# Kernel optimization log

Measured on AMD Instinct MI355X. Metric: run time of the kernel, lower is better.

## Reference

```python
import jax, jax.numpy as jnp
import numpy as np

B, N, D, H, L = 1024, 31, 576, 16, 12   # batch, tokens (30 patches + cls), dim, heads, depth
DH = D // H        # 36 head dim
FF = 4 * D         # 2304 mlp hidden
NC = 1000          # num_classes
EPS = 1e-5         # torch nn.LayerNorm default
NEG = -987654321.0 # exact constant used for the LSA diagonal mask


def layer_norm(x, w, b):
    m = jnp.mean(x, axis=-1, keepdims=True)
    v = jnp.mean((x - m) ** 2, axis=-1, keepdims=True)
    return (x - m) * jax.lax.rsqrt(v + EPS) * w + b


def setup_inputs() -> dict:
    key = jax.random.key(0)
    ks = jax.random.split(key, 12)
    s = 0.02
    return {
        "x": jax.random.normal(ks[0], (B, N, D), jnp.float32),
        # per-layer stacked params (scanned over depth L)
        "qkv_w": jax.random.normal(ks[1], (L, 3 * D, D), jnp.float32) * s,
        "scale": (DH ** -0.5) * jnp.ones((L, H), jnp.float32),  # learnable per-head LSA scale
        "out_w": jax.random.normal(ks[2], (L, D, D), jnp.float32) * s,
        "out_b": jnp.zeros((L, D), jnp.float32),
        "ln1_w": jnp.ones((L, D), jnp.float32),
        "ln1_b": jnp.zeros((L, D), jnp.float32),
        "ln2_w": jnp.ones((L, D), jnp.float32),
        "ln2_b": jnp.zeros((L, D), jnp.float32),
        "fc1_w": jax.random.normal(ks[3], (L, FF, D), jnp.float32) * s,
        "fc1_b": jnp.zeros((L, FF), jnp.float32),
        "fc2_w": jax.random.normal(ks[4], (L, D, FF), jnp.float32) * s,
        "fc2_b": jnp.zeros((L, D), jnp.float32),
        "norm_w": jnp.ones((D,), jnp.float32),
        "norm_b": jnp.zeros((D,), jnp.float32),
        "head_w": jax.random.normal(ks[5], (NC, D), jnp.float32) * s,
        "head_b": jnp.zeros((NC,), jnp.float32),
    }


def reference(x, qkv_w, scale, out_w, out_b, ln1_w, ln1_b, ln2_w, ln2_b,
              fc1_w, fc1_b, fc2_w, fc2_b, norm_w, norm_b, head_w, head_b):
    diag = jnp.eye(N, dtype=bool)  # LSA diagonal mask (self-token)

    def block(h, p):
        qw, sc, ow, ob, w1, b1, w2, b2, g1, be1, g2, be2 = p
        # --- LSA attention ---
        y = layer_norm(h, g1, be1)
        qkv = jnp.einsum('bnd,ed->bne', y, qw)            # [B,N,3D]
        q, k, v = jnp.split(qkv, 3, axis=-1)
        to_heads = lambda t: t.reshape(t.shape[0], N, H, DH).transpose(0, 2, 1, 3)
        q, k, v = to_heads(q), to_heads(k), to_heads(v)   # [B,H,N,DH]
        dots = jnp.einsum('bhid,bhjd->bhij', q, k) * sc[None, :, None, None]
        dots = jnp.where(diag, NEG, dots)                 # diagonal -> -987654321
        attn = jax.nn.softmax(dots, axis=-1)
        o = jnp.einsum('bhij,bhjd->bhid', attn, v)
        o = o.transpose(0, 2, 1, 3).reshape(h.shape[0], N, D)
        h = h + jnp.einsum('bnd,ed->bne', o, ow) + ob
        # --- MLP (exact GELU) ---
        y = layer_norm(h, g2, be2)
        m = jax.nn.gelu(jnp.einsum('bnd,fd->bnf', y, w1) + b1, approximate=False)
        h = h + jnp.einsum('bnf,df->bnd', m, w2) + b2
        return h, None

    params = (qkv_w, scale, out_w, out_b, fc1_w, fc1_b, fc2_w, fc2_b,
              ln1_w, ln1_b, ln2_w, ln2_b)
    x, _ = jax.lax.scan(block, x, params)
    x = layer_norm(x, norm_w, norm_b)
    cls = x[:, 0]                                         # cls token
    return cls @ head_w.T + head_b                        # [B, NC]
```

## Files before the change

kernel.cpp:

```cpp
#include <hip/hip_runtime.h>
#include <stdint.h>

typedef unsigned short u16;
typedef __bf16 bf16x8 __attribute__((ext_vector_type(8)));
typedef float f32x4 __attribute__((ext_vector_type(4)));

#define B_   1024
#define N_   31
#define D_   576
#define H_   16
#define L_   12
#define DH_  36
#define FF_  2304
#define NC_  1000
#define M_   (B_*N_)
#define NEG_ (-987654321.0f)

__device__ __forceinline__ u16 f2bfbits(float f) {
  uint32_t x = __builtin_bit_cast(uint32_t, f);
  x += 0x7fffu + ((x >> 16) & 1u);
  return (u16)(x >> 16);
}
__device__ __forceinline__ float bfbits2f(u16 u) {
  return __builtin_bit_cast(float, (uint32_t)u << 16);
}
__device__ __forceinline__ float lo_bf(uint32_t w) {
  return __builtin_bit_cast(float, w << 16);
}
__device__ __forceinline__ float hi_bf(uint32_t w) {
  return __builtin_bit_cast(float, w & 0xffff0000u);
}

typedef __attribute__((address_space(1))) void gvoid_t;
typedef __attribute__((address_space(3))) void lvoid_t;
__device__ __forceinline__ void async16(void* lds, const void* g) {
  __builtin_amdgcn_global_load_lds((gvoid_t*)const_cast<void*>(g), (lvoid_t*)lds, 16, 0, 0);
}

template<int EPI>
__global__ __launch_bounds__(256, 3)
void gemm_bt(const u16* __restrict__ A, const u16* __restrict__ Bw,
             int N, int K,
             const float* __restrict__ bias,
             float* __restrict__ resid,
             u16* __restrict__ outb,
             float* __restrict__ outf, int Nreal)
{
  __shared__ alignas(16) u16 As[256 * 32];
  __shared__ alignas(16) u16 Bs[64 * 32];

  const int t    = threadIdx.x;
  const int wave = t >> 6;
  const int lane = t & 63;

  const int nwg  = gridDim.x * gridDim.y;
  const int orig = blockIdx.y * gridDim.x + blockIdx.x;
  const int q = nwg >> 3, r = nwg & 7, xc = orig & 7, o = orig >> 3;
  const int wid = (xc < r ? xc * (q + 1) : r * (q + 1) + (xc - r) * q) + o;
  const int mBase = (wid / gridDim.x) * 256;
  const int nBase = (wid % gridDim.x) * 64;

  const int tr = t >> 2;
  const int tc = (t & 3) * 8;

  const int fr = lane & 15;
  const int fk = (lane >> 4) * 8;
  const u16* aBase = &As[(wave * 64 + fr) * 32 + fk];
  const u16* bBase = &Bs[fr * 32 + fk];

  f32x4 acc[4][4] = {};

  for (int k0 = 0; k0 < K; k0 += 32) {
    #pragma unroll
    for (int i = 0; i < 4; ++i) {
      int row = i * 64 + tr;
      async16(&As[row * 32 + tc], A + (long)(mBase + row) * K + k0 + tc);
    }
    async16(&Bs[tr * 32 + tc], Bw + (long)(nBase + tr) * K + k0 + tc);
    asm volatile("s_waitcnt vmcnt(0)" ::: "memory");
    __syncthreads();

    bf16x8 af[4], bf_[4];
    #pragma unroll
    for (int m = 0; m < 4; ++m) af[m]  = *(const bf16x8*)(aBase + m * 16 * 32);
    #pragma unroll
    for (int n = 0; n < 4; ++n) bf_[n] = *(const bf16x8*)(bBase + n * 16 * 32);
    #pragma unroll
    for (int m = 0; m < 4; ++m)
      #pragma unroll
      for (int n = 0; n < 4; ++n)
        acc[m][n] = __builtin_amdgcn_mfma_f32_16x16x32_bf16(af[m], bf_[n], acc[m][n], 0, 0, 0);
    __syncthreads();
  }

  const int fq = lane >> 4;
  #pragma unroll
  for (int m = 0; m < 4; ++m) {
    int gr0 = mBase + wave * 64 + m * 16 + fq * 4;
    #pragma unroll
    for (int n = 0; n < 4; ++n) {
      int gc = nBase + n * 16 + fr;
      #pragma unroll
      for (int r2 = 0; r2 < 4; ++r2) {
        long gr = gr0 + r2;
        float v = acc[m][n][r2];
        if (EPI == 0) {
          outb[gr * N + gc] = f2bfbits(v);
        } else if (EPI == 1) {
          long idx = gr * N + gc;
          resid[idx] = resid[idx] + v + bias[gc];
        } else if (EPI == 2) {
          float x = v + bias[gc];
          float g = 0.5f * x * (1.0f + erff(x * 0.70710678118654752f));
          outb[gr * N + gc] = f2bfbits(g);
        } else {
          if (gc < Nreal) outf[gr * Nreal + gc] = v + bias[gc];
        }
      }
    }
  }
}

__global__ __launch_bounds__(256)
void ln_kernel(const float* __restrict__ x, long tokStride,
               const float* __restrict__ w, const float* __restrict__ b,
               u16* __restrict__ y)
{
  int tok  = blockIdx.x * 4 + (threadIdx.x >> 6);
  int lane = threadIdx.x & 63;
  const float* row = x + (long)tok * tokStride;
  float v[9]; float s = 0.f, sq = 0.f;
  #pragma unroll
  for (int j = 0; j < 9; ++j) { v[j] = row[lane + j * 64]; s += v[j]; sq += v[j] * v[j]; }
  #pragma unroll
  for (int o = 32; o; o >>= 1) { s += __shfl_xor(s, o); sq += __shfl_xor(sq, o); }
  float mean = s * (1.f / 576.f);
  float var  = sq * (1.f / 576.f) - mean * mean;
  float inv  = rsqrtf(var + 1e-5f);
  u16* yr = y + (long)tok * 576;
  #pragma unroll
  for (int j = 0; j < 9; ++j) {
    int c = lane + j * 64;
    yr[c] = f2bfbits((v[j] - mean) * inv * w[c] + b[c]);
  }
}

__global__ __launch_bounds__(256)
void attn_kernel(const u16* __restrict__ qkv, u16* __restrict__ o,
                 const float* __restrict__ scale)
{
  __shared__ float kls[4][N_ * DH_];
  __shared__ float vls[4][N_ * DH_];
  int wave = threadIdx.x >> 6, lane = threadIdx.x & 63;
  int bh = blockIdx.x * 4 + wave;
  int b  = bh >> 4, h = bh & 15;
  long base = (long)b * N_ * 1728 + h * DH_;

  for (int u = lane; u < 558; u += 64) {
    int row = u / 18, c = (u % 18) * 2;
    uint32_t kw = *(const uint32_t*)(qkv + base + 576  + (long)row * 1728 + c);
    uint32_t vw = *(const uint32_t*)(qkv + base + 1152 + (long)row * 1728 + c);
    kls[wave][row * 36 + c]     = lo_bf(kw);
    kls[wave][row * 36 + c + 1] = hi_bf(kw);
    vls[wave][row * 36 + c]     = lo_bf(vw);
    vls[wave][row * 36 + c + 1] = hi_bf(vw);
  }
  __syncthreads();

  int i0 = lane >> 1, p = lane & 1;
  int i  = i0 > 30 ? 30 : i0;
  float qv[18];
  const u16* qrow = qkv + base + (long)i * 1728 + p * 18;
  #pragma unroll
  for (int d = 0; d < 18; ++d) qv[d] = bfbits2f(qrow[d]);

  float s[31];
  #pragma unroll
  for (int j = 0; j < 31; ++j) {
    float a = 0.f;
    const float* kr = &kls[wave][j * 36 + p * 18];
    #pragma unroll
    for (int d = 0; d < 18; ++d) a += qv[d] * kr[d];
    a += __shfl_xor(a, 1);
    s[j] = a;
  }
  float sc = scale[h];
  float mx = -1e30f;
  #pragma unroll
  for (int j = 0; j < 31; ++j) { s[j] = (j == i) ? NEG_ : s[j] * sc; mx = fmaxf(mx, s[j]); }
  float sum = 0.f;
  #pragma unroll
  for (int j = 0; j < 31; ++j) { s[j] = expf(s[j] - mx); sum += s[j]; }
  float inv = 1.f / sum;

  #pragma unroll
  for (int d = 0; d < 18; ++d) {
    float a = 0.f;
    #pragma unroll
    for (int j = 0; j < 31; ++j) a += s[j] * vls[wave][j * 36 + p * 18 + d];
    if (i0 < 31)
      o[(long)(b * N_ + i0) * 576 + h * DH_ + p * 18 + d] = f2bfbits(a * inv);
  }
}

__global__ void cvt_layer(const float4* __restrict__ s0, const float4* __restrict__ s1,
                          const float4* __restrict__ s2, const float4* __restrict__ s3,
                          u16* __restrict__ d0, u16* __restrict__ d1,
                          u16* __restrict__ d2, u16* __restrict__ d3)
{
  int idx = blockIdx.x * 256 + threadIdx.x;
  const float4* s; u16* d; int off;
  if (idx < 248832)      { s = s0; d = d0; off = idx; }
  else if (idx < 331776) { s = s1; d = d1; off = idx - 248832; }
  else if (idx < 663552) { s = s2; d = d2; off = idx - 331776; }
  else                   { s = s3; d = d3; off = idx - 663552; }
  float4 v = s[off];
  ushort4 r;
  r.x = f2bfbits(v.x); r.y = f2bfbits(v.y); r.z = f2bfbits(v.z); r.w = f2bfbits(v.w);
  *(ushort4*)(d + (long)off * 4) = r;
}

__global__ void pad_head(const float* __restrict__ hw, u16* __restrict__ out)
{
  int idx = blockIdx.x * 256 + threadIdx.x;
  int row = idx / 576;
  out[idx] = (row < NC_) ? f2bfbits(hw[idx]) : (u16)0;
}

extern "C" void kernel_launch(void* const* d_in, const int* in_sizes, int n_in,
                              void* d_out, int out_size, void* d_ws, size_t ws_size,
                              hipStream_t stream)
{
  (void)in_sizes; (void)n_in; (void)out_size;
  const float* x      = (const float*)d_in[0];
  const float* qkv_w  = (const float*)d_in[1];
  const float* scale  = (const float*)d_in[2];
  const float* out_w  = (const float*)d_in[3];
  const float* out_b  = (const float*)d_in[4];
  const float* ln1_w  = (const float*)d_in[5];
  const float* ln1_b  = (const float*)d_in[6];
  const float* ln2_w  = (const float*)d_in[7];
  const float* ln2_b  = (const float*)d_in[8];
  const float* fc1_w  = (const float*)d_in[9];
  const float* fc1_b  = (const float*)d_in[10];
  const float* fc2_w  = (const float*)d_in[11];
  const float* fc2_b  = (const float*)d_in[12];
  const float* norm_w = (const float*)d_in[13];
  const float* norm_b = (const float*)d_in[14];
  const float* head_w = (const float*)d_in[15];
  const float* head_b = (const float*)d_in[16];

  auto al = [](size_t b) { return (b + 255) & ~(size_t)255; };
  const size_t fixed = al((size_t)M_ * D_ * 4) + al((size_t)M_ * D_ * 2)
                     + al((size_t)1728 * D_ * 2) + al((size_t)D_ * D_ * 2)
                     + al((size_t)FF_ * D_ * 2) + al((size_t)D_ * FF_ * 2)
                     + 2 * al((size_t)1024 * D_ * 2);
  const size_t cbuf2 = al((size_t)(M_ / 2) * FF_ * 2);
  const int nch = (ws_size >= fixed + cbuf2) ? 2 : 4;
  const int MC  = M_ / nch;
  const int BCc = B_ / nch;

  char* p = (char*)d_ws;
  auto take = [&](size_t bytes) { char* r = p; p += (bytes + 255) & ~(size_t)255; return r; };
  float* h    = (float*)take((size_t)M_ * D_ * 4);
  u16*   ybuf = (u16*)take((size_t)M_ * D_ * 2);
  u16*   cbuf = (u16*)take((size_t)MC * FF_ * 2);
  u16*   wq_l = (u16*)take((size_t)1728 * D_ * 2);
  u16*   wo_l = (u16*)take((size_t)D_ * D_ * 2);
  u16*   w1_l = (u16*)take((size_t)FF_ * D_ * 2);
  u16*   w2_l = (u16*)take((size_t)D_ * FF_ * 2);
  u16*   whead = (u16*)take((size_t)1024 * D_ * 2);
  u16*   cls   = (u16*)take((size_t)1024 * D_ * 2);

  pad_head<<<(1024 * 576) / 256, 256, 0, stream>>>(head_w, whead);
  hipMemcpyAsync(h, x, (size_t)M_ * D_ * 4, hipMemcpyDeviceToDevice, stream);

  for (int l = 0; l < L_; ++l) {
    cvt_layer<<<3888, 256, 0, stream>>>(
        (const float4*)(qkv_w + (size_t)l * 1728 * D_),
        (const float4*)(out_w + (size_t)l * D_ * D_),
        (const float4*)(fc1_w + (size_t)l * FF_ * D_),
        (const float4*)(fc2_w + (size_t)l * D_ * FF_),
        wq_l, wo_l, w1_l, w2_l);

    ln_kernel<<<M_ / 4, 256, 0, stream>>>(h, 576, ln1_w + l * D_, ln1_b + l * D_, ybuf);
    for (int c = 0; c < nch; ++c) {
      long off = (long)c * MC;
      gemm_bt<0><<<dim3(1728 / 64, MC / 256), 256, 0, stream>>>(
          ybuf + off * D_, wq_l, 1728, 576, nullptr, nullptr, cbuf, nullptr, 0);
      attn_kernel<<<(BCc * H_) / 4, 256, 0, stream>>>(cbuf, ybuf + off * D_, scale + l * H_);
    }
    gemm_bt<1><<<dim3(576 / 64, M_ / 256), 256, 0, stream>>>(
        ybuf, wo_l, 576, 576, out_b + l * D_, h, nullptr, nullptr, 0);

    ln_kernel<<<M_ / 4, 256, 0, stream>>>(h, 576, ln2_w + l * D_, ln2_b + l * D_, ybuf);
    for (int c = 0; c < nch; ++c) {
      long off = (long)c * MC;
      gemm_bt<2><<<dim3(FF_ / 64, MC / 256), 256, 0, stream>>>(
          ybuf + off * D_, w1_l, 2304, 576, fc1_b + l * FF_, nullptr, cbuf, nullptr, 0);
      gemm_bt<1><<<dim3(576 / 64, MC / 256), 256, 0, stream>>>(
          cbuf, w2_l, 576, 2304, fc2_b + l * D_, h + off * D_, nullptr, nullptr, 0);
    }
  }
  ln_kernel<<<1024 / 4, 256, 0, stream>>>(h, (long)N_ * 576, norm_w, norm_b, cls);
  gemm_bt<3><<<dim3(1024 / 64, 1024 / 256), 256, 0, stream>>>(
      cls, whead, 1024, 576, head_b, nullptr, nullptr, (float*)d_out, NC_);
}
```

Baseline: 7.625 ms.

## Add XOR-swizzled LDS layout and 128-row tiles for narrow-N GEMMs

The GEMM kernel is templated on the M tile size. The N=576 GEMMs (out-proj, fc2, head) switch to 128-row tiles with a 2x2 wave layout, which doubles the workgroup count for those launches. The global-to-LDS copies and the fragment reads also gain an XOR swizzle on the k-chunk index, meant to cut LDS bank conflicts on the 16-byte MFMA fragment loads. Smaller tiles lower per-block reuse of the A and B tiles, and the swizzle adds a little index arithmetic.

Result: no change. 7.586 ms (-0.5%).

```diff
diff --git a/kernel.cpp b/kernel.cpp
--- a/kernel.cpp
+++ b/kernel.cpp
@@ -37,7 +37,7 @@
   __builtin_amdgcn_global_load_lds((gvoid_t*)const_cast<void*>(g), (lvoid_t*)lds, 16, 0, 0);
 }
 
-template<int EPI>
+template<int EPI, int BM>
 __global__ __launch_bounds__(256, 3)
 void gemm_bt(const u16* __restrict__ A, const u16* __restrict__ Bw,
              int N, int K,
@@ -46,7 +46,8 @@
              u16* __restrict__ outb,
              float* __restrict__ outf, int Nreal)
 {
-  __shared__ alignas(16) u16 As[256 * 32];
+  constexpr int NF = (BM == 256) ? 4 : 2;
+  __shared__ alignas(16) u16 As[BM * 32];
   __shared__ alignas(16) u16 Bs[64 * 32];
 
   const int t    = threadIdx.x;
@@ -57,38 +58,41 @@
   const int orig = blockIdx.y * gridDim.x + blockIdx.x;
   const int q = nwg >> 3, r = nwg & 7, xc = orig & 7, o = orig >> 3;
   const int wid = (xc < r ? xc * (q + 1) : r * (q + 1) + (xc - r) * q) + o;
-  const int mBase = (wid / gridDim.x) * 256;
+  const int mBase = (wid / gridDim.x) * BM;
   const int nBase = (wid % gridDim.x) * 64;
 
+  const int wm   = (BM == 256) ? wave : (wave >> 1);
+  const int wcol = (BM == 256) ? 0 : (wave & 1) * 32;
+
   const int tr = t >> 2;
-  const int tc = (t & 3) * 8;
+  const int tc = ((t & 3) ^ ((t >> 3) & 3)) * 8;
 
   const int fr = lane & 15;
-  const int fk = (lane >> 4) * 8;
-  const u16* aBase = &As[(wave * 64 + fr) * 32 + fk];
-  const u16* bBase = &Bs[fr * 32 + fk];
-
-  f32x4 acc[4][4] = {};
+  const int fk = (((lane >> 4) ^ ((lane >> 1) & 3))) * 8;
+  const u16* aBase = &As[(wm * 64 + fr) * 32 + fk];
+  const u16* bBase = &Bs[(wcol + fr) * 32 + fk];
+
+  f32x4 acc[4][NF] = {};
 
   for (int k0 = 0; k0 < K; k0 += 32) {
     #pragma unroll
-    for (int i = 0; i < 4; ++i) {
+    for (int i = 0; i < BM / 64; ++i) {
       int row = i * 64 + tr;
-      async16(&As[row * 32 + tc], A + (long)(mBase + row) * K + k0 + tc);
+      async16(&As[row * 32 + (t & 3) * 8], A + (long)(mBase + row) * K + k0 + tc);
     }
-    async16(&Bs[tr * 32 + tc], Bw + (long)(nBase + tr) * K + k0 + tc);
+    async16(&Bs[tr * 32 + (t & 3) * 8], Bw + (long)(nBase + tr) * K + k0 + tc);
     asm volatile("s_waitcnt vmcnt(0)" ::: "memory");
     __syncthreads();
 
-    bf16x8 af[4], bf_[4];
+    bf16x8 af[4], bf_[NF];
     #pragma unroll
     for (int m = 0; m < 4; ++m) af[m]  = *(const bf16x8*)(aBase + m * 16 * 32);
     #pragma unroll
-    for (int n = 0; n < 4; ++n) bf_[n] = *(const bf16x8*)(bBase + n * 16 * 32);
+    for (int n = 0; n < NF; ++n) bf_[n] = *(const bf16x8*)(bBase + n * 16 * 32);
     #pragma unroll
     for (int m = 0; m < 4; ++m)
       #pragma unroll
-      for (int n = 0; n < 4; ++n)
+      for (int n = 0; n < NF; ++n)
         acc[m][n] = __builtin_amdgcn_mfma_f32_16x16x32_bf16(af[m], bf_[n], acc[m][n], 0, 0, 0);
     __syncthreads();
   }
@@ -96,10 +100,10 @@
   const int fq = lane >> 4;
   #pragma unroll
   for (int m = 0; m < 4; ++m) {
-    int gr0 = mBase + wave * 64 + m * 16 + fq * 4;
-    #pragma unroll
-    for (int n = 0; n < 4; ++n) {
-      int gc = nBase + n * 16 + fr;
+    int gr0 = mBase + wm * 64 + m * 16 + fq * 4;
+    #pragma unroll
+    for (int n = 0; n < NF; ++n) {
+      int gc = nBase + wcol + n * 16 + fr;
       #pragma unroll
       for (int r2 = 0; r2 < 4; ++r2) {
         long gr = gr0 + r2;
@@ -286,23 +290,23 @@
     ln_kernel<<<M_ / 4, 256, 0, stream>>>(h, 576, ln1_w + l * D_, ln1_b + l * D_, ybuf);
     for (int c = 0; c < nch; ++c) {
       long off = (long)c * MC;
-      gemm_bt<0><<<dim3(1728 / 64, MC / 256), 256, 0, stream>>>(
+      gemm_bt<0, 256><<<dim3(1728 / 64, MC / 256), 256, 0, stream>>>(
           ybuf + off * D_, wq_l, 1728, 576, nullptr, nullptr, cbuf, nullptr, 0);
       attn_kernel<<<(BCc * H_) / 4, 256, 0, stream>>>(cbuf, ybuf + off * D_, scale + l * H_);
     }
-    gemm_bt<1><<<dim3(576 / 64, M_ / 256), 256, 0, stream>>>(
+    gemm_bt<1, 128><<<dim3(576 / 64, M_ / 128), 256, 0, stream>>>(
         ybuf, wo_l, 576, 576, out_b + l * D_, h, nullptr, nullptr, 0);
 
     ln_kernel<<<M_ / 4, 256, 0, stream>>>(h, 576, ln2_w + l * D_, ln2_b + l * D_, ybuf);
     for (int c = 0; c < nch; ++c) {
       long off = (long)c * MC;
-      gemm_bt<2><<<dim3(FF_ / 64, MC / 256), 256, 0, stream>>>(
+      gemm_bt<2, 256><<<dim3(FF_ / 64, MC / 256), 256, 0, stream>>>(
           ybuf + off * D_, w1_l, 2304, 576, fc1_b + l * FF_, nullptr, cbuf, nullptr, 0);
-      gemm_bt<1><<<dim3(576 / 64, MC / 256), 256, 0, stream>>>(
+      gemm_bt<1, 128><<<dim3(576 / 64, MC / 128), 256, 0, stream>>>(
           cbuf, w2_l, 576, 2304, fc2_b + l * D_, h + off * D_, nullptr, nullptr, 0);
     }
   }
   ln_kernel<<<1024 / 4, 256, 0, stream>>>(h, (long)N_ * 576, norm_w, norm_b, cls);
-  gemm_bt<3><<<dim3(1024 / 64, 1024 / 256), 256, 0, stream>>>(
+  gemm_bt<3, 128><<<dim3(1024 / 64, 1024 / 128), 256, 0, stream>>>(
       cls, whead, 1024, 576, head_b, nullptr, nullptr, (float*)d_out, NC_);
 }
```
